# Kernel optimization log

Measured on AMD Instinct MI355X. Metric: run time of the kernel, lower is better.

The kernel has to match this reference:

```python
import jax, jax.numpy as jnp
import numpy as np

N = 50000      # nodes
E = 800000     # edges (avg degree 16)
D = 64         # num_hidden
H = 4          # heads
OUT = 64       # out_dim

def setup_inputs() -> dict:
    key = jax.random.key(0)
    k = jax.random.split(key, 5)
    h = jax.random.normal(k[0], (N, D), dtype=jnp.float32)
    edge_index = jax.random.randint(k[1], (2, E), 0, N)
    gate_w = jax.random.normal(k[2], (H, 2 * D), dtype=jnp.float32) * 0.1  # per-head gate Linear weight
    gate_b = jnp.zeros((H,), dtype=jnp.float32)
    W_cat = jax.random.normal(k[3], (OUT, H * D), dtype=jnp.float32) * 0.05
    b_cat = jnp.zeros((OUT,), dtype=jnp.float32)
    return dict(h=h, edge_index=edge_index, gate_w=gate_w, gate_b=gate_b, W_cat=W_cat, b_cat=b_cat)

def reference(h, edge_index, gate_w, gate_b, W_cat, b_cat):
    # eval mode: both dropouts are identity
    row, col = edge_index[0], edge_index[1]
    n, d = h.shape
    # symmetric-ish degree normalization based on out-degree of row (as in original)
    deg = jax.ops.segment_sum(jnp.ones((row.shape[0],), dtype=h.dtype), row, num_segments=n)
    nd = jnp.clip(deg, 1.0) ** -0.5                     # [N]
    hr = h[row]                                          # [E, D] gather (source)
    hc = h[col]                                          # [E, D] gather (target)
    # per-head gate: tanh(Linear(cat(hr, hc))) vectorized over heads
    w1 = gate_w[:, :d]                                   # [H, D]
    w2 = gate_w[:, d:]                                   # [H, D]
    g = jnp.tanh(hr @ w1.T + hc @ w2.T + gate_b)        # [E, H]
    norm = g * (nd[row] * nd[col])[:, None]              # [E, H]
    # message: norm * x_j where x_j = h[source] = hr; aggregate (add) at target = col
    msgs = norm[:, :, None] * hr[:, None, :]             # [E, H, D]
    agg = jax.ops.segment_sum(msgs, col, num_segments=n) # [N, H, D]
    res = agg.reshape(n, -1)                             # concat heads -> [N, H*D]
    return jax.nn.relu(res @ W_cat.T + b_cat)            # [N, OUT]
```

## Files before the change

kernel.cpp:

```cpp
#include <hip/hip_runtime.h>

#define DD 64
#define HH 4
#define OUTC 64
#define CAP 48
#define CHUNK 4096

typedef __attribute__((ext_vector_type(8))) short bf16x8;
typedef __attribute__((ext_vector_type(4))) float f32x4;

__device__ __forceinline__ float fast_tanh(float x) {
    x = fminf(fmaxf(x, -15.f), 15.f);
    float e = __expf(2.f * x);
    return 1.f - 2.f / (e + 1.f);
}

__device__ __forceinline__ float bcast_f(float v, int k) {
    return __uint_as_float(__builtin_amdgcn_readlane(__float_as_uint(v), k));
}
__device__ __forceinline__ int bcast_i(int v, int k) {
    return __builtin_amdgcn_readlane(v, k);
}

__device__ __forceinline__ unsigned short f2bf(float f) {
    unsigned int u = __float_as_uint(f);
    u = (u + 0x7FFFu + ((u >> 16) & 1u)) >> 16;
    return (unsigned short)u;
}
__device__ __forceinline__ float bfld(const unsigned short* p) {
    return __uint_as_float(((unsigned)*p) << 16);
}

__global__ __launch_bounds__(256) void partition_kernel(const int* __restrict__ row,
                                                        const int* __restrict__ col,
                                                        unsigned* __restrict__ cbuck,
                                                        unsigned char* __restrict__ rbuck,
                                                        int* __restrict__ ccount,
                                                        int* __restrict__ rcount,
                                                        int E, int NBUK, int BCAP, int nchunks) {
    __shared__ int hist[256];
    __shared__ int scn[256];
    __shared__ int gbase[256];
    __shared__ unsigned stage[CHUNK];
    __shared__ int saddr[CHUNK];
    int tid = threadIdx.x;
    int phaseC = (blockIdx.x < nchunks) ? 1 : 0;
    int chunk = phaseC ? blockIdx.x : blockIdx.x - nchunks;
    int e0 = chunk * CHUNK;
    int n = E - e0;
    if (n > CHUNK) n = CHUNK;
    const int* key = phaseC ? col : row;

    hist[tid] = 0;
    __syncthreads();
    for (int i = tid; i < n; i += 256) atomicAdd(&hist[key[e0 + i] >> 8], 1);
    __syncthreads();
    int v = hist[tid];
    scn[tid] = v;
    __syncthreads();
    for (int d = 1; d < 256; d <<= 1) {
        int a = (tid >= d) ? scn[tid - d] : 0;
        __syncthreads();
        scn[tid] += a;
        __syncthreads();
    }
    int excl = scn[tid] - v;
    scn[tid] = excl;
    if (tid < NBUK && v > 0)
        gbase[tid] = tid * BCAP + atomicAdd(phaseC ? &ccount[tid] : &rcount[tid], v);
    else
        gbase[tid] = tid * BCAP;
    hist[tid] = 0;
    __syncthreads();

    if (phaseC) {
        for (int i = tid; i < n; i += 256) {
            int c = col[e0 + i];
            int r = row[e0 + i];
            int b = c >> 8;
            int k = atomicAdd(&hist[b], 1);
            int p = scn[b] + k;
            stage[p] = ((unsigned)r << 8) | (unsigned)(c & 255);
            saddr[p] = gbase[b] + k;
        }
        __syncthreads();
        for (int i = tid; i < n; i += 256) cbuck[saddr[i]] = stage[i];
    } else {
        unsigned char* stB = (unsigned char*)stage;
        for (int i = tid; i < n; i += 256) {
            int r = row[e0 + i];
            int b = r >> 8;
            int k = atomicAdd(&hist[b], 1);
            int p = scn[b] + k;
            stB[p] = (unsigned char)(r & 255);
            saddr[p] = gbase[b] + k;
        }
        __syncthreads();
        for (int i = tid; i < n; i += 256) rbuck[saddr[i]] = stB[i];
    }
}

#define HSTR 68
__global__ __launch_bounds__(256) void local_prep(const unsigned* __restrict__ cbuck,
                                                  const unsigned char* __restrict__ rbuck,
                                                  const int* __restrict__ ccount,
                                                  const int* __restrict__ rcount,
                                                  int* __restrict__ cnt,
                                                  unsigned short* __restrict__ slots,
                                                  float* __restrict__ nd,
                                                  const float* __restrict__ h,
                                                  const float* __restrict__ gate_w,
                                                  const float* __restrict__ gate_b,
                                                  float* __restrict__ a12,
                                                  unsigned short* __restrict__ hbs,
                                                  int N, int NBUK, int BCAP) {
    __shared__ int cur[256];
    __shared__ float hs[256 * HSTR];
    __shared__ float gws[8 * 64];
    __shared__ float ndf[256];
    int tid = threadIdx.x;
    int b = blockIdx.x;
    cur[tid] = 0;
    __syncthreads();
    if (b < NBUK) {
        int s = ccount[b];
        if (s > BCAP) s = BCAP;
        const unsigned* src = cbuck + (size_t)b * BCAP;
        int node0 = b << 8;
        for (int i = tid; i < s; i += 256) {
            unsigned rc = src[i];
            int cl = rc & 255;
            int r = (int)(rc >> 8);
            int k = atomicAdd(&cur[cl], 1);
            if (k < CAP) slots[(size_t)(node0 + cl) * CAP + k] = (unsigned short)r;
        }
        __syncthreads();
        int node = node0 + tid;
        if (node < N) cnt[node] = cur[tid];
    } else {
        int bb = b - NBUK;
        int node0 = bb << 8;
        int nn = N - node0;
        if (nn > 256) nn = 256;
        int s = rcount[bb];
        if (s > BCAP) s = BCAP;
        const unsigned char* src = rbuck + (size_t)bb * BCAP;
        for (int i = tid; i < s; i += 256) atomicAdd(&cur[src[i]], 1);
        for (int i = tid; i < 512; i += 256) gws[i] = gate_w[i];
        int tile4 = nn * 16;
        const float4* hsrc = (const float4*)(h + (size_t)node0 * DD);
        for (int i = tid; i < tile4; i += 256) {
            int j = i >> 4, q = i & 15;
            *(float4*)&hs[j * HSTR + q * 4] = hsrc[i];
        }
        __syncthreads();
        int node = node0 + tid;
        if (tid < nn) {
            int dg = cur[tid];
            float ndv = rsqrtf((float)(dg < 1 ? 1 : dg));
            nd[node] = ndv;
            ndf[tid] = ndv;
        }
        __syncthreads();
        if (tid < nn) {
            float acc[8];
#pragma unroll
            for (int m = 0; m < 8; ++m) acc[m] = 0.f;
            const float4* hrow = (const float4*)&hs[tid * HSTR];
#pragma unroll
            for (int q = 0; q < 16; ++q) {
                float4 hv = hrow[q];
#pragma unroll
                for (int m = 0; m < 8; ++m) {
                    float4 gv = *(const float4*)&gws[m * 64 + q * 4];
                    acc[m] += hv.x * gv.x + hv.y * gv.y + hv.z * gv.z + hv.w * gv.w;
                }
            }
#pragma unroll
            for (int m = 0; m < 8; ++m) {
                int hd = m >> 1, part = m & 1;
                float vv = acc[m] + (part == 0 ? gate_b[hd] : 0.f);
                a12[(size_t)node * 8 + part * 4 + hd] = vv;
            }
        }
        for (int i = tid; i < tile4; i += 256) {
            int j = i >> 4, q = i & 15;
            float sc = ndf[j];
            const float* p = &hs[j * HSTR + q * 4];
            ushort4 pv;
            pv.x = f2bf(sc * p[0]);
            pv.y = f2bf(sc * p[1]);
            pv.z = f2bf(sc * p[2]);
            pv.w = f2bf(sc * p[3]);
            *(ushort4*)&hbs[(size_t)(node0 + j) * DD + q * 4] = pv;
        }
    }
}

__global__ __launch_bounds__(256) void gather_kernel(const int* __restrict__ cnt,
                                                     const unsigned short* __restrict__ slots,
                                                     const float* __restrict__ nd,
                                                     const float* __restrict__ a12,
                                                     const unsigned short* __restrict__ hbs,
                                                     unsigned short* __restrict__ aggb, int N) {
    int lane = threadIdx.x & 63;
    int gwave = (blockIdx.x * blockDim.x + threadIdx.x) >> 6;
    int nwaves = (gridDim.x * blockDim.x) >> 6;
    const unsigned short* hl = hbs + lane;
    for (int c0 = gwave * 2; c0 < N; c0 += nwaves * 2) {
        int c1 = c0 + 1;
        bool has1 = (c1 < N);
        int len0 = cnt[c0];
        if (len0 > CAP) len0 = CAP;
        int len1 = has1 ? cnt[c1] : 0;
        if (len1 > CAP) len1 = CAP;
        float nd0 = nd[c0];
        float nd1 = has1 ? nd[c1] : 0.f;
        float4 a2_0 = *(const float4*)&a12[(size_t)c0 * 8 + 4];
        float4 a2_1 = has1 ? *(const float4*)&a12[(size_t)c1 * 8 + 4] : make_float4(0, 0, 0, 0);
        int r0 = 0, r1 = 0;
        float t00 = 0.f, t01 = 0.f, t02 = 0.f, t03 = 0.f;
        float t10 = 0.f, t11 = 0.f, t12 = 0.f, t13 = 0.f;
        if (lane < len0) {
            r0 = slots[(size_t)c0 * CAP + lane];
            float4 a1 = *(const float4*)&a12[(size_t)r0 * 8];
            t00 = fast_tanh(a1.x + a2_0.x);
            t01 = fast_tanh(a1.y + a2_0.y);
            t02 = fast_tanh(a1.z + a2_0.z);
            t03 = fast_tanh(a1.w + a2_0.w);
        }
        if (lane < len1) {
            r1 = slots[(size_t)c1 * CAP + lane];
            float4 a1 = *(const float4*)&a12[(size_t)r1 * 8];
            t10 = fast_tanh(a1.x + a2_1.x);
            t11 = fast_tanh(a1.y + a2_1.y);
            t12 = fast_tanh(a1.z + a2_1.z);
            t13 = fast_tanh(a1.w + a2_1.w);
        }
        float b00 = 0.f, b01 = 0.f, b02 = 0.f, b03 = 0.f;
        float b10 = 0.f, b11 = 0.f, b12 = 0.f, b13 = 0.f;
        int L0 = (len0 + 7) & ~7;
        int L1 = (len1 + 7) & ~7;
        int L = L0 > L1 ? L0 : L1;
        for (int j = 0; j < L; j += 8) {
            float fv0[8], fv1[8];
            bool d0 = (j < L0), d1 = (j < L1);
            if (d0) {
#pragma unroll
                for (int u = 0; u < 8; ++u) {
                    int rj = bcast_i(r0, j + u);
                    fv0[u] = bfld(hl + ((size_t)rj << 6));
                }
            }
            if (d1) {
#pragma unroll
                for (int u = 0; u < 8; ++u) {
                    int rj = bcast_i(r1, j + u);
                    fv1[u] = bfld(hl + ((size_t)rj << 6));
                }
            }
            if (d0) {
#pragma unroll
                for (int u = 0; u < 8; ++u) {
                    b00 += bcast_f(t00, j + u) * fv0[u];
                    b01 += bcast_f(t01, j + u) * fv0[u];
                    b02 += bcast_f(t02, j + u) * fv0[u];
                    b03 += bcast_f(t03, j + u) * fv0[u];
                }
            }
            if (d1) {
#pragma unroll
                for (int u = 0; u < 8; ++u) {
                    b10 += bcast_f(t10, j + u) * fv1[u];
                    b11 += bcast_f(t11, j + u) * fv1[u];
                    b12 += bcast_f(t12, j + u) * fv1[u];
                    b13 += bcast_f(t13, j + u) * fv1[u];
                }
            }
        }
        size_t o = (size_t)c0 * 256 + lane;
        aggb[o] = f2bf(b00 * nd0);
        aggb[o + 64] = f2bf(b01 * nd0);
        aggb[o + 128] = f2bf(b02 * nd0);
        aggb[o + 192] = f2bf(b03 * nd0);
        if (has1) {
            size_t o1 = (size_t)c1 * 256 + lane;
            aggb[o1] = f2bf(b10 * nd1);
            aggb[o1 + 64] = f2bf(b11 * nd1);
            aggb[o1 + 128] = f2bf(b12 * nd1);
            aggb[o1 + 192] = f2bf(b13 * nd1);
        }
    }
}

__global__ __launch_bounds__(256) void gemm_kernel(const unsigned short* __restrict__ aggb,
                                                   const float* __restrict__ Wcat,
                                                   const float* __restrict__ b_cat,
                                                   float* __restrict__ out, int N) {
    __shared__ unsigned short WT[2048 * 8];
    int tid = threadIdx.x;
#pragma unroll
    for (int it = 0; it < 8; ++it) {
        int id = tid + it * 256;
        int ln = id & 63;
        int ks = (id >> 6) & 7;
        int ct = id >> 9;
        int o = ct * 16 + (ln & 15);
        int kb = ks * 32 + ((ln >> 4) & 3) * 8;
        const float4* src = (const float4*)&Wcat[(size_t)o * 256 + kb];
        float4 w0 = src[0];
        float4 w1 = src[1];
        ushort4* dst = (ushort4*)&WT[(size_t)id * 8];
        dst[0] = make_ushort4(f2bf(w0.x), f2bf(w0.y), f2bf(w0.z), f2bf(w0.w));
        dst[1] = make_ushort4(f2bf(w1.x), f2bf(w1.y), f2bf(w1.z), f2bf(w1.w));
    }
    __syncthreads();

    int lane = tid & 63;
    int wv = tid >> 6;
    int m = lane & 15;
    int q = lane >> 4;
    float bb[4];
#pragma unroll
    for (int ct = 0; ct < 4; ++ct) bb[ct] = b_cat[ct * 16 + m];

    int ntiles = (N + 15) >> 4;
    int wgid = blockIdx.x * 4 + wv;
    int nwaves = gridDim.x * 4;
    for (int tile = wgid; tile < ntiles; tile += nwaves) {
        int n0 = tile << 4;
        int node = n0 + m;
        bf16x8 afrag[8];
        bool ok = (node < N);
        const unsigned short* arow = aggb + (size_t)node * 256 + q * 8;
#pragma unroll
        for (int ks = 0; ks < 8; ++ks) {
            if (ok)
                afrag[ks] = *(const bf16x8*)(arow + ks * 32);
            else
                afrag[ks] = (bf16x8)(short)0;
        }
        f32x4 acc[4];
#pragma unroll
        for (int ct = 0; ct < 4; ++ct) acc[ct] = (f32x4){0.f, 0.f, 0.f, 0.f};
#pragma unroll
        for (int ks = 0; ks < 8; ++ks) {
#pragma unroll
            for (int ct = 0; ct < 4; ++ct) {
                bf16x8 bfrag = *(const bf16x8*)&WT[(size_t)((ct * 8 + ks) * 64 + lane) * 8];
                acc[ct] = __builtin_amdgcn_mfma_f32_16x16x32_bf16(afrag[ks], bfrag, acc[ct], 0, 0, 0);
            }
        }
#pragma unroll
        for (int reg = 0; reg < 4; ++reg) {
            int n = n0 + q * 4 + reg;
            if (n < N) {
#pragma unroll
                for (int ct = 0; ct < 4; ++ct) {
                    float v = acc[ct][reg] + bb[ct];
                    out[(size_t)n * OUTC + ct * 16 + m] = v > 0.f ? v : 0.f;
                }
            }
        }
    }
}

extern "C" void kernel_launch(void* const* d_in, const int* in_sizes, int n_in,
                              void* d_out, int out_size, void* d_ws, size_t ws_size,
                              hipStream_t stream) {
    const float* h      = (const float*)d_in[0];
    const int*   edge   = (const int*)d_in[1];
    const float* gate_w = (const float*)d_in[2];
    const float* gate_b = (const float*)d_in[3];
    const float* Wcat   = (const float*)d_in[4];
    const float* b_cat  = (const float*)d_in[5];
    int N = in_sizes[0] / DD;
    int E = in_sizes[1] / 2;
    const int* row = edge;
    const int* colp = edge + E;
    float* out = (float*)d_out;

    int NBUK = (N + 255) >> 8;
    int BCAP = ((2 * E / NBUK) + 63) & ~63;

    char* ws = (char*)d_ws;
    size_t off = 0;
    size_t pad = ((size_t)NBUK * 4 + 255) & ~255ull;
    int*   ccount = (int*)(ws + off); off += pad;
    int*   rcount = (int*)(ws + off); off += pad;
    int*   cnt    = (int*)(ws + off); off += (size_t)N * 4;
    float* nd     = (float*)(ws + off); off += (size_t)N * 4;
    float* a12    = (float*)(ws + off); off += (size_t)N * 32;
    unsigned short* slots = (unsigned short*)(ws + off); off += ((size_t)N * CAP * 2 + 255) & ~255ull;
    unsigned short* hbs  = (unsigned short*)(ws + off); off += (size_t)N * DD * 2;
    unsigned short* aggb = (unsigned short*)(ws + off);
    unsigned*      cbuck = (unsigned*)aggb;
    unsigned char* rbuck = (unsigned char*)((char*)aggb + (size_t)NBUK * BCAP * 4);

    hipMemsetAsync(ccount, 0, pad + (size_t)NBUK * 4, stream);

    int nchunks = (E + CHUNK - 1) / CHUNK;
    partition_kernel<<<2 * nchunks, 256, 0, stream>>>(row, colp, cbuck, rbuck, ccount, rcount,
                                                      E, NBUK, BCAP, nchunks);
    local_prep<<<2 * NBUK, 256, 0, stream>>>(cbuck, rbuck, ccount, rcount, cnt, slots, nd,
                                             h, gate_w, gate_b, a12, hbs, N, NBUK, BCAP);
    gather_kernel<<<3125, 256, 0, stream>>>(cnt, slots, nd, a12, hbs, aggb, N);
    gemm_kernel<<<256, 256, 0, stream>>>(aggb, Wcat, b_cat, out, N);
}
```

Before: 164.0 us.

## Recast per-node gated gather-aggregate as bf16 MFMA over 4-node groups

The gather kernel now handles groups of four destination nodes per wave. Edge gates are packed into a block-diagonal bf16 A matrix in LDS, and the aggregation is done with 16x16x32 bf16 MFMA instructions, with neighbor feature rows gathered as the B operand. This replaces the readlane-broadcast scalar FMA loop, which aimed to cut VALU and readlane overhead. In exchange it adds LDS zero-fill and staging, rounds the gates to bf16, and does scattered 2-byte gathers per lane for the B fragments, which may be less coalesced than the previous row-contiguous loads.

```diff
diff --git a/kernel.cpp b/kernel.cpp
--- a/kernel.cpp
+++ b/kernel.cpp
@@ -15,20 +15,10 @@
     return 1.f - 2.f / (e + 1.f);
 }
 
-__device__ __forceinline__ float bcast_f(float v, int k) {
-    return __uint_as_float(__builtin_amdgcn_readlane(__float_as_uint(v), k));
-}
-__device__ __forceinline__ int bcast_i(int v, int k) {
-    return __builtin_amdgcn_readlane(v, k);
-}
-
 __device__ __forceinline__ unsigned short f2bf(float f) {
     unsigned int u = __float_as_uint(f);
     u = (u + 0x7FFFu + ((u >> 16) & 1u)) >> 16;
     return (unsigned short)u;
-}
-__device__ __forceinline__ float bfld(const unsigned short* p) {
-    return __uint_as_float(((unsigned)*p) << 16);
 }
 
 __global__ __launch_bounds__(256) void partition_kernel(const int* __restrict__ row,
@@ -203,92 +193,85 @@
                                                      const float* __restrict__ a12,
                                                      const unsigned short* __restrict__ hbs,
                                                      unsigned short* __restrict__ aggb, int N) {
-    int lane = threadIdx.x & 63;
-    int gwave = (blockIdx.x * blockDim.x + threadIdx.x) >> 6;
+    __shared__ char lds[4 * 6912];
+    int tid = threadIdx.x;
+    int wv = tid >> 6;
+    int lane = tid & 63;
+    int quad = lane >> 4;
+    int mcol = lane & 15;
+    char* Alds = lds + wv * 6912;
+    unsigned short* Au = (unsigned short*)Alds;
+    int* rlds = (int*)(Alds + 6144);
+
+    int gwave = (blockIdx.x * blockDim.x + tid) >> 6;
     int nwaves = (gridDim.x * blockDim.x) >> 6;
-    const unsigned short* hl = hbs + lane;
-    for (int c0 = gwave * 2; c0 < N; c0 += nwaves * 2) {
-        int c1 = c0 + 1;
-        bool has1 = (c1 < N);
-        int len0 = cnt[c0];
-        if (len0 > CAP) len0 = CAP;
-        int len1 = has1 ? cnt[c1] : 0;
-        if (len1 > CAP) len1 = CAP;
-        float nd0 = nd[c0];
-        float nd1 = has1 ? nd[c1] : 0.f;
-        float4 a2_0 = *(const float4*)&a12[(size_t)c0 * 8 + 4];
-        float4 a2_1 = has1 ? *(const float4*)&a12[(size_t)c1 * 8 + 4] : make_float4(0, 0, 0, 0);
-        int r0 = 0, r1 = 0;
-        float t00 = 0.f, t01 = 0.f, t02 = 0.f, t03 = 0.f;
-        float t10 = 0.f, t11 = 0.f, t12 = 0.f, t13 = 0.f;
-        if (lane < len0) {
-            r0 = slots[(size_t)c0 * CAP + lane];
-            float4 a1 = *(const float4*)&a12[(size_t)r0 * 8];
-            t00 = fast_tanh(a1.x + a2_0.x);
-            t01 = fast_tanh(a1.y + a2_0.y);
-            t02 = fast_tanh(a1.z + a2_0.z);
-            t03 = fast_tanh(a1.w + a2_0.w);
-        }
-        if (lane < len1) {
-            r1 = slots[(size_t)c1 * CAP + lane];
-            float4 a1 = *(const float4*)&a12[(size_t)r1 * 8];
-            t10 = fast_tanh(a1.x + a2_1.x);
-            t11 = fast_tanh(a1.y + a2_1.y);
-            t12 = fast_tanh(a1.z + a2_1.z);
-            t13 = fast_tanh(a1.w + a2_1.w);
-        }
-        float b00 = 0.f, b01 = 0.f, b02 = 0.f, b03 = 0.f;
-        float b10 = 0.f, b11 = 0.f, b12 = 0.f, b13 = 0.f;
-        int L0 = (len0 + 7) & ~7;
-        int L1 = (len1 + 7) & ~7;
-        int L = L0 > L1 ? L0 : L1;
-        for (int j = 0; j < L; j += 8) {
-            float fv0[8], fv1[8];
-            bool d0 = (j < L0), d1 = (j < L1);
-            if (d0) {
-#pragma unroll
-                for (int u = 0; u < 8; ++u) {
-                    int rj = bcast_i(r0, j + u);
-                    fv0[u] = bfld(hl + ((size_t)rj << 6));
-                }
-            }
-            if (d1) {
-#pragma unroll
-                for (int u = 0; u < 8; ++u) {
-                    int rj = bcast_i(r1, j + u);
-                    fv1[u] = bfld(hl + ((size_t)rj << 6));
-                }
-            }
-            if (d0) {
-#pragma unroll
-                for (int u = 0; u < 8; ++u) {
-                    b00 += bcast_f(t00, j + u) * fv0[u];
-                    b01 += bcast_f(t01, j + u) * fv0[u];
-                    b02 += bcast_f(t02, j + u) * fv0[u];
-                    b03 += bcast_f(t03, j + u) * fv0[u];
-                }
-            }
-            if (d1) {
-#pragma unroll
-                for (int u = 0; u < 8; ++u) {
-                    b10 += bcast_f(t10, j + u) * fv1[u];
-                    b11 += bcast_f(t11, j + u) * fv1[u];
-                    b12 += bcast_f(t12, j + u) * fv1[u];
-                    b13 += bcast_f(t13, j + u) * fv1[u];
-                }
-            }
-        }
-        size_t o = (size_t)c0 * 256 + lane;
-        aggb[o] = f2bf(b00 * nd0);
-        aggb[o + 64] = f2bf(b01 * nd0);
-        aggb[o + 128] = f2bf(b02 * nd0);
-        aggb[o + 192] = f2bf(b03 * nd0);
-        if (has1) {
-            size_t o1 = (size_t)c1 * 256 + lane;
-            aggb[o1] = f2bf(b10 * nd1);
-            aggb[o1 + 64] = f2bf(b11 * nd1);
-            aggb[o1 + 128] = f2bf(b12 * nd1);
-            aggb[o1 + 192] = f2bf(b13 * nd1);
+    int ngroups = (N + 3) >> 2;
+
+    for (int g = gwave; g < ngroups; g += nwaves) {
+        int c0 = g << 2;
+        int o0 = 0, o1, o2, o3, o4;
+        {
+            int l0 = (c0 + 0 < N) ? cnt[c0 + 0] : 0; if (l0 > CAP) l0 = CAP;
+            int l1 = (c0 + 1 < N) ? cnt[c0 + 1] : 0; if (l1 > CAP) l1 = CAP;
+            int l2 = (c0 + 2 < N) ? cnt[c0 + 2] : 0; if (l2 > CAP) l2 = CAP;
+            int l3 = (c0 + 3 < N) ? cnt[c0 + 3] : 0; if (l3 > CAP) l3 = CAP;
+            o1 = l0; o2 = o1 + l1; o3 = o2 + l2; o4 = o3 + l3;
+        }
+        int K = o4;
+        int ksteps = (K + 31) >> 5;
+        for (int z = lane; z < ksteps * 256; z += 64) ((unsigned*)Au)[z] = 0u;
+        for (int z = lane; z < ksteps * 32; z += 64) rlds[z] = 0;
+        for (int p = lane; p < K; p += 64) {
+            int i = (p >= o1) + (p >= o2) + (p >= o3);
+            int c = c0 + i;
+            int off = p - (i == 0 ? 0 : (i == 1 ? o1 : (i == 2 ? o2 : o3)));
+            int r = slots[(size_t)c * CAP + off];
+            rlds[p] = r;
+            float4 a1 = *(const float4*)&a12[(size_t)r * 8];
+            float4 a2 = *(const float4*)&a12[(size_t)c * 8 + 4];
+            float t0 = fast_tanh(a1.x + a2.x);
+            float t1 = fast_tanh(a1.y + a2.y);
+            float t2 = fast_tanh(a1.z + a2.z);
+            float t3 = fast_tanh(a1.w + a2.w);
+            int bidx = (p >> 5) * 512 + ((p >> 3) & 3) * 128 + (p & 7);
+            int m0 = i * 4;
+            Au[bidx + (m0 + 0) * 8] = f2bf(t0);
+            Au[bidx + (m0 + 1) * 8] = f2bf(t1);
+            Au[bidx + (m0 + 2) * 8] = f2bf(t2);
+            Au[bidx + (m0 + 3) * 8] = f2bf(t3);
+        }
+        f32x4 acc0 = (f32x4){0.f, 0.f, 0.f, 0.f};
+        f32x4 acc1 = (f32x4){0.f, 0.f, 0.f, 0.f};
+        f32x4 acc2 = (f32x4){0.f, 0.f, 0.f, 0.f};
+        f32x4 acc3 = (f32x4){0.f, 0.f, 0.f, 0.f};
+        for (int ks = 0; ks < ksteps; ++ks) {
+            bf16x8 af = *(const bf16x8*)(Alds + ks * 1024 + lane * 16);
+            int rk[8];
+#pragma unroll
+            for (int j = 0; j < 8; ++j) rk[j] = rlds[ks * 32 + quad * 8 + j];
+#pragma unroll
+            for (int nt = 0; nt < 4; ++nt) {
+                const unsigned short* hp = hbs + nt * 16 + mcol;
+                bf16x8 bf;
+#pragma unroll
+                for (int j = 0; j < 8; ++j) bf[j] = (short)hp[(size_t)rk[j] << 6];
+                if (nt == 0) acc0 = __builtin_amdgcn_mfma_f32_16x16x32_bf16(af, bf, acc0, 0, 0, 0);
+                else if (nt == 1) acc1 = __builtin_amdgcn_mfma_f32_16x16x32_bf16(af, bf, acc1, 0, 0, 0);
+                else if (nt == 2) acc2 = __builtin_amdgcn_mfma_f32_16x16x32_bf16(af, bf, acc2, 0, 0, 0);
+                else acc3 = __builtin_amdgcn_mfma_f32_16x16x32_bf16(af, bf, acc3, 0, 0, 0);
+            }
+        }
+        int node = c0 + quad;
+        if (node < N) {
+            float ndv = nd[node];
+            unsigned short* dst = aggb + (size_t)node * 256 + mcol;
+#pragma unroll
+            for (int reg = 0; reg < 4; ++reg) {
+                dst[reg * 64 + 0] = f2bf(acc0[reg] * ndv);
+                dst[reg * 64 + 16] = f2bf(acc1[reg] * ndv);
+                dst[reg * 64 + 32] = f2bf(acc2[reg] * ndv);
+                dst[reg * 64 + 48] = f2bf(acc3[reg] * ndv);
+            }
         }
     }
 }
```

Measured after the change: 146.0 us. -11.0%, faster.
